# Kernel tuning notes

Hardware: AMD Instinct MI355X
Metric: run time of the kernel (lower is better)

Reference implementation:

```python
import jax, jax.numpy as jnp
import numpy as np

B, N, C, H = 2, 2048, 768, 12
D = C // H            # head_dim = 64
SCALE = D ** -0.5
QMAX_8 = 127.0        # int8 symmetric weights/activations (BIT_TYPE_W / BIT_TYPE_A)
LOG_QMAX = 15.0       # uint4 log-domain softmax (BIT_TYPE_S)


def setup_inputs() -> dict:
    key = jax.random.key(0)
    k0, k1, k2 = jax.random.split(key, 3)
    x = jax.random.normal(k0, (B, N, C), jnp.float32)
    w_qkv = jax.random.normal(k1, (3 * C, C), jnp.float32) * 0.02
    b_qkv = jnp.zeros((3 * C,), jnp.float32)
    w_out = jax.random.normal(k2, (C, C), jnp.float32) * 0.02
    b_out = jnp.zeros((C,), jnp.float32)
    return {"x": x, "w_qkv": w_qkv, "b_qkv": b_qkv, "w_out": w_out, "b_out": b_out}


def fake_quant_sym(t):
    """Symmetric per-tensor int8 fake-quantize (quantize->dequantize), STE for grads."""
    s = jnp.max(jnp.abs(t)) / QMAX_8 + 1e-8
    deq = jnp.clip(jnp.round(t / s), -QMAX_8, QMAX_8) * s
    return t + jax.lax.stop_gradient(deq - t)


def log_int_softmax(attn):
    """Log-int-softmax: softmax then 4-bit log2 quantization, attn_q = 2^{-round(-log2 p)}."""
    p = jax.nn.softmax(attn, axis=-1)
    lg = jnp.clip(jnp.round(-jnp.log2(jnp.maximum(p, 2.0 ** -24))), 0.0, LOG_QMAX)
    q = jnp.exp2(-lg)
    return p + jax.lax.stop_gradient(q - p)


def reference(x, w_qkv, b_qkv, w_out, b_out):
    # QLinear: fake-quantized weight GEMM
    qkv = x @ fake_quant_sym(w_qkv).T + b_qkv            # [B,N,3C]
    qkv = fake_quant_sym(qkv)                            # qact_qkv
    qkv = qkv.reshape(B, N, 3, H, D).transpose(2, 0, 3, 1, 4)  # [3,B,H,N,D]
    q, k, v = qkv[0], qkv[1], qkv[2]
    attn = jnp.einsum("bhnd,bhmd->bhnm", q, k) * SCALE   # [B,H,N,N]
    attn = fake_quant_sym(attn)                          # qact_attn
    p = log_int_softmax(attn)
    o = jnp.einsum("bhnm,bhmd->bhnd", p, v)              # [B,H,N,D]
    o = o.transpose(0, 2, 1, 3).reshape(B, N, C)
    out = o @ fake_quant_sym(w_out).T + b_out            # out_proj (QLinear)
    out = fake_quant_sym(out)                            # qact_out
    return out
```

## Files before the change

kernel.cpp:

```cpp
#include <hip/hip_runtime.h>

#define NB 2
#define NN 2048
#define NC 768
#define NH 12
#define ND 64
#define ROWS (NB * NN)
#define K3C (3 * NC)
#define NHEADS (NB * NH)
#define ATTN_SCALE 0.125f

typedef __attribute__((ext_vector_type(8))) short s16x8;
typedef __attribute__((ext_vector_type(4))) float f32x4;
typedef __attribute__((ext_vector_type(2))) unsigned int u32x2;

__device__ __forceinline__ float qsc(const unsigned* u) {
    return __uint_as_float(*u) / 127.0f + 1e-8f;
}
__device__ __forceinline__ float fq(float t, float s) {
    return fminf(fmaxf(rintf(t / s), -127.0f), 127.0f) * s;
}
__device__ __forceinline__ float qcode(float t, float s) {
    return fminf(fmaxf(rintf(t / s), -127.0f), 127.0f);
}
__device__ __forceinline__ short bfbits(float f) {
    return (short)(__float_as_uint(f) >> 16);
}
__device__ __forceinline__ ushort bf_rne(float x) {
    unsigned u = __float_as_uint(x);
    return (ushort)((u + 0x7fffu + ((u >> 16) & 1u)) >> 16);
}

__global__ __launch_bounds__(256) void maxabs_kernel(const float* __restrict__ x,
                                                     long long n, unsigned* out) {
    float m = 0.0f;
    long long stride4 = (long long)gridDim.x * blockDim.x * 4;
    for (long long j = ((long long)blockIdx.x * blockDim.x + threadIdx.x) * 4; j < n; j += stride4) {
        float4 v = *(const float4*)(x + j);
        m = fmaxf(m, fmaxf(fmaxf(fabsf(v.x), fabsf(v.y)), fmaxf(fabsf(v.z), fabsf(v.w))));
    }
    for (int off = 32; off > 0; off >>= 1) m = fmaxf(m, __shfl_down(m, off, 64));
    __shared__ float sm[4];
    int lane = threadIdx.x & 63, w = threadIdx.x >> 6;
    if (lane == 0) sm[w] = m;
    __syncthreads();
    if (threadIdx.x == 0) {
        float mm = fmaxf(fmaxf(sm[0], sm[1]), fmaxf(sm[2], sm[3]));
        atomicMax(out, __float_as_uint(mm));
    }
}

__global__ __launch_bounds__(256) void quant_kernel(const float* in, float* out,
                                                    long long n, const unsigned* umax) {
    float s = qsc(umax);
    long long stride4 = (long long)gridDim.x * blockDim.x * 4;
    for (long long j = ((long long)blockIdx.x * blockDim.x + threadIdx.x) * 4; j < n; j += stride4) {
        float4 v = *(const float4*)(in + j);
        v.x = fq(v.x, s); v.y = fq(v.y, s); v.z = fq(v.z, s); v.w = fq(v.w, s);
        *(float4*)(out + j) = v;
    }
}

__global__ __launch_bounds__(256) void quantcodes_kernel(const float* __restrict__ in,
                                                         ushort* __restrict__ codes,
                                                         long long n,
                                                         const unsigned* __restrict__ umax) {
    float s = qsc(umax);
    long long stride8 = (long long)gridDim.x * blockDim.x * 8;
    for (long long j = ((long long)blockIdx.x * blockDim.x + threadIdx.x) * 8; j < n; j += stride8) {
        float4 a = *(const float4*)(in + j);
        float4 b = *(const float4*)(in + j + 4);
        s16x8 o;
        o[0] = bfbits(qcode(a.x, s)); o[1] = bfbits(qcode(a.y, s));
        o[2] = bfbits(qcode(a.z, s)); o[3] = bfbits(qcode(a.w, s));
        o[4] = bfbits(qcode(b.x, s)); o[5] = bfbits(qcode(b.y, s));
        o[6] = bfbits(qcode(b.z, s)); o[7] = bfbits(qcode(b.w, s));
        *(s16x8*)(codes + j) = o;
    }
}

__global__ __launch_bounds__(256) void split3_kernel(const float* __restrict__ in,
                                                     ushort* __restrict__ xs,
                                                     long long n) {
    long long stride8 = (long long)gridDim.x * blockDim.x * 8;
    for (long long j = ((long long)blockIdx.x * blockDim.x + threadIdx.x) * 8; j < n; j += stride8) {
        long long row = j / NC, col = j % NC;
        s16x8 h, m, l;
#pragma unroll
        for (int i = 0; i < 8; i += 4) {
            float4 v = *(const float4*)(in + j + i);
            float vv[4] = {v.x, v.y, v.z, v.w};
#pragma unroll
            for (int t = 0; t < 4; ++t) {
                ushort hb = bf_rne(vv[t]);
                float hf = __uint_as_float(((unsigned)hb) << 16);
                float r1 = vv[t] - hf;
                ushort mb = bf_rne(r1);
                float mf = __uint_as_float(((unsigned)mb) << 16);
                h[i + t] = (short)hb;
                m[i + t] = (short)mb;
                l[i + t] = (short)bf_rne(r1 - mf);
            }
        }
        ushort* dst = xs + row * (3 * NC) + col;
        *(s16x8*)(dst) = h;
        *(s16x8*)(dst + NC) = m;
        *(s16x8*)(dst + 2 * NC) = l;
    }
}

__global__ __launch_bounds__(256) void gemm3_mfma_kernel(const ushort* __restrict__ As,
                                                         const ushort* __restrict__ Bc,
                                                         const float* __restrict__ bias,
                                                         float* __restrict__ Cm, int Nn,
                                                         const unsigned* __restrict__ uB,
                                                         unsigned* __restrict__ uC) {
    __shared__ ushort ah[128 * 64], am[128 * 64], al[128 * 64], bs[128 * 64];
    __shared__ float redmx[4];
    const float sB = qsc(uB);
    const int tid = threadIdx.x, l = tid & 63, w = tid >> 6;
    const int row0 = blockIdx.y * 128, col0 = blockIdx.x * 128;
    const int wr = w >> 1, wc = w & 1;
    f32x4 acc[4][4];
#pragma unroll
    for (int m = 0; m < 4; ++m)
#pragma unroll
        for (int n = 0; n < 4; ++n) acc[m][n] = (f32x4){0.f, 0.f, 0.f, 0.f};

    const int sr = tid >> 1, sh = (tid & 1) << 5;
    const int su = sh >> 3, s7 = sr & 7;

    for (int k0 = 0; k0 < NC; k0 += 64) {
        __syncthreads();
        {
            const ushort* ph = As + (size_t)(row0 + sr) * (3 * NC) + k0 + sh;
            ushort* dsts[3] = {ah + sr * 64, am + sr * 64, al + sr * 64};
#pragma unroll
            for (int pl = 0; pl < 3; ++pl) {
                const ushort* p = ph + pl * NC;
                s16x8 t0 = *(const s16x8*)(p),      t1 = *(const s16x8*)(p + 8);
                s16x8 t2 = *(const s16x8*)(p + 16), t3 = *(const s16x8*)(p + 24);
                ushort* d = dsts[pl];
                *(s16x8*)(d + (((su | 0) ^ s7) << 3)) = t0;
                *(s16x8*)(d + (((su | 1) ^ s7) << 3)) = t1;
                *(s16x8*)(d + (((su | 2) ^ s7) << 3)) = t2;
                *(s16x8*)(d + (((su | 3) ^ s7) << 3)) = t3;
            }
            const ushort* pb = Bc + (size_t)(col0 + sr) * NC + k0 + sh;
            s16x8 b0 = *(const s16x8*)(pb),      b1 = *(const s16x8*)(pb + 8);
            s16x8 b2 = *(const s16x8*)(pb + 16), b3 = *(const s16x8*)(pb + 24);
            ushort* brow = bs + sr * 64;
            *(s16x8*)(brow + (((su | 0) ^ s7) << 3)) = b0;
            *(s16x8*)(brow + (((su | 1) ^ s7) << 3)) = b1;
            *(s16x8*)(brow + (((su | 2) ^ s7) << 3)) = b2;
            *(s16x8*)(brow + (((su | 3) ^ s7) << 3)) = b3;
        }
        __syncthreads();
#pragma unroll
        for (int ks = 0; ks < 2; ++ks) {
            s16x8 bf[4];
#pragma unroll
            for (int n = 0; n < 4; ++n) {
                int br = wc * 64 + n * 16 + (l & 15);
                bf[n] = *(s16x8*)(bs + br * 64 + ((((ks << 2) + (l >> 4)) ^ (br & 7)) << 3));
            }
#pragma unroll
            for (int m = 0; m < 4; ++m) {
                int ar = wr * 64 + m * 16 + (l & 15);
                int ao = ar * 64 + ((((ks << 2) + (l >> 4)) ^ (ar & 7)) << 3);
                s16x8 af = *(s16x8*)(ah + ao);
                s16x8 mf_ = *(s16x8*)(am + ao);
                s16x8 ef = *(s16x8*)(al + ao);
#pragma unroll
                for (int n = 0; n < 4; ++n) {
                    acc[m][n] = __builtin_amdgcn_mfma_f32_16x16x32_bf16(af, bf[n], acc[m][n], 0, 0, 0);
                    acc[m][n] = __builtin_amdgcn_mfma_f32_16x16x32_bf16(mf_, bf[n], acc[m][n], 0, 0, 0);
                    acc[m][n] = __builtin_amdgcn_mfma_f32_16x16x32_bf16(ef, bf[n], acc[m][n], 0, 0, 0);
                }
            }
        }
    }
    float mx = 0.0f;
#pragma unroll
    for (int n = 0; n < 4; ++n) {
        int col = col0 + wc * 64 + n * 16 + (l & 15);
        float bv = bias[col];
#pragma unroll
        for (int m = 0; m < 4; ++m) {
            int grow = row0 + wr * 64 + m * 16 + ((l >> 4) << 2);
#pragma unroll
            for (int r = 0; r < 4; ++r) {
                float v = fmaf(sB, acc[m][n][r], bv);
                Cm[(size_t)(grow + r) * Nn + col] = v;
                mx = fmaxf(mx, fabsf(v));
            }
        }
    }
    for (int msk = 1; msk < 64; msk <<= 1) mx = fmaxf(mx, __shfl_xor(mx, msk, 64));
    if (l == 0) redmx[w] = mx;
    __syncthreads();
    if (tid == 0)
        atomicMax(uC, __float_as_uint(fmaxf(fmaxf(redmx[0], redmx[1]), fmaxf(redmx[2], redmx[3]))));
}

__device__ __forceinline__ void stage_k_tile(const ushort* __restrict__ src,
                                             ushort* lds, int tid) {
    int row = tid >> 2, u0 = (tid & 3) << 1, r7 = row & 7;
    const ushort* p = src + (size_t)row * K3C + (u0 << 3);
    s16x8 t0 = *(const s16x8*)(p);
    s16x8 t1 = *(const s16x8*)(p + 8);
    *(s16x8*)(lds + row * 64 + ((u0 ^ r7) << 3)) = t0;
    *(s16x8*)(lds + row * 64 + (((u0 | 1) ^ r7) << 3)) = t1;
}

__device__ __forceinline__ void stage_vT_tile(const ushort* __restrict__ src,
                                              ushort* lds, int tid) {
    int j = tid >> 2, d0 = (tid & 3) << 4;
    const ushort* p = src + (size_t)j * K3C + d0;
    s16x8 a = *(const s16x8*)(p);
    s16x8 b = *(const s16x8*)(p + 8);
    int jo = j >> 3, jl = j & 7;
#pragma unroll
    for (int t = 0; t < 8; ++t) {
        int d = d0 + t;
        lds[d * 64 + ((jo ^ (d & 7)) << 3) + jl] = (ushort)a[t];
    }
#pragma unroll
    for (int t = 0; t < 8; ++t) {
        int d = d0 + 8 + t;
        lds[d * 64 + ((jo ^ (d & 7)) << 3) + jl] = (ushort)b[t];
    }
}

__global__ __launch_bounds__(256) void attn_maxdot_kernel(const ushort* __restrict__ codes,
                                                          unsigned* __restrict__ umaxdot) {
    __shared__ ushort kt[64 * 64];
    __shared__ float red[4];
    int bh = blockIdx.y, b = bh / NH, h = bh % NH;
    int i0 = blockIdx.x * 64;
    int tid = threadIdx.x, l = tid & 63, w = tid >> 6;
    int qr = l & 15, g = l >> 4;

    const ushort* qp = codes + (size_t)(b * NN + i0 + w * 16 + qr) * K3C + h * ND + (g << 3);
    s16x8 qf0 = *(const s16x8*)(qp);
    s16x8 qf1 = *(const s16x8*)(qp + 32);

    const ushort* kbase = codes + (size_t)(b * NN) * K3C + NC + h * ND;
    float md = 0.0f;
    for (int st = 0; st < NN / 64; ++st) {
        __syncthreads();
        stage_k_tile(kbase + (size_t)st * 64 * K3C, kt, tid);
        __syncthreads();
#pragma unroll
        for (int jt = 0; jt < 4; ++jt) {
            int row = (jt << 4) + qr;
            f32x4 acc = {0.f, 0.f, 0.f, 0.f};
            s16x8 kf0 = *(s16x8*)(kt + row * 64 + (((g    ) ^ (row & 7)) << 3));
            s16x8 kf1 = *(s16x8*)(kt + row * 64 + (((g + 4) ^ (row & 7)) << 3));
            acc = __builtin_amdgcn_mfma_f32_16x16x32_bf16(kf0, qf0, acc, 0, 0, 0);
            acc = __builtin_amdgcn_mfma_f32_16x16x32_bf16(kf1, qf1, acc, 0, 0, 0);
#pragma unroll
            for (int r = 0; r < 4; ++r) md = fmaxf(md, fabsf(acc[r]));
        }
    }
    for (int m = 1; m < 64; m <<= 1) md = fmaxf(md, __shfl_xor(md, m, 64));
    if (l == 0) red[w] = md;
    __syncthreads();
    if (tid == 0)
        atomicMax(umaxdot, __float_as_uint(fmaxf(fmaxf(red[0], red[1]), fmaxf(red[2], red[3]))));
}

__global__ __launch_bounds__(256) void attn_fused_kernel(const ushort* __restrict__ codes,
                                                         const unsigned* __restrict__ uq,
                                                         const unsigned* __restrict__ umaxdot,
                                                         float* __restrict__ O) {
    __shared__ ushort kt[64 * 64];
    __shared__ ushort vt[64 * 64];
    __shared__ ushort ps[4][16 * 64];
    int bh = blockIdx.y, b = bh / NH, h = bh % NH;
    int i0 = blockIdx.x * 64;
    int tid = threadIdx.x, l = tid & 63, w = tid >> 6;
    int qr = l & 15, g = l >> 4;
    float s = qsc(uq);
    float cf = s * s * ATTN_SCALE;
    float sa = __uint_as_float(*umaxdot) * cf / 127.0f + 1e-8f;
    float rr = cf / sa;
    float kk = sa * 1.44269504088896340736f;

    const ushort* qp = codes + (size_t)(b * NN + i0 + w * 16 + qr) * K3C + h * ND + (g << 3);
    s16x8 qf0 = *(const s16x8*)(qp);
    s16x8 qf1 = *(const s16x8*)(qp + 32);

    const ushort* kbase = codes + (size_t)(b * NN) * K3C + NC + h * ND;
    const ushort* vbase = codes + (size_t)(b * NN) * K3C + 2 * NC + h * ND;

    float U = 0.0f;
    for (int st = 0; st < NN / 64; ++st) {
        __syncthreads();
        stage_k_tile(kbase + (size_t)st * 64 * K3C, kt, tid);
        __syncthreads();
#pragma unroll
        for (int jt = 0; jt < 4; ++jt) {
            int row = (jt << 4) + qr;
            f32x4 acc = {0.f, 0.f, 0.f, 0.f};
            s16x8 kf0 = *(s16x8*)(kt + row * 64 + (((g    ) ^ (row & 7)) << 3));
            s16x8 kf1 = *(s16x8*)(kt + row * 64 + (((g + 4) ^ (row & 7)) << 3));
            acc = __builtin_amdgcn_mfma_f32_16x16x32_bf16(kf0, qf0, acc, 0, 0, 0);
            acc = __builtin_amdgcn_mfma_f32_16x16x32_bf16(kf1, qf1, acc, 0, 0, 0);
#pragma unroll
            for (int r = 0; r < 4; ++r) {
                float m = rintf(acc[r] * rr);
                U += exp2f(kk * m);
            }
        }
    }
    U += __shfl_xor(U, 16, 64);
    U += __shfl_xor(U, 32, 64);
    float lu = log2f(U);

    f32x4 oacc[4];
#pragma unroll
    for (int dt = 0; dt < 4; ++dt) oacc[dt] = (f32x4){0.f, 0.f, 0.f, 0.f};
    ushort* myps = (ushort*)ps[w];
    for (int st = 0; st < NN / 64; ++st) {
        __syncthreads();
        stage_k_tile(kbase + (size_t)st * 64 * K3C, kt, tid);
        stage_vT_tile(vbase + (size_t)st * 64 * K3C, vt, tid);
        __syncthreads();
#pragma unroll
        for (int jt = 0; jt < 4; ++jt) {
            int row = (jt << 4) + qr;
            f32x4 acc = {0.f, 0.f, 0.f, 0.f};
            s16x8 kf0 = *(s16x8*)(kt + row * 64 + (((g    ) ^ (row & 7)) << 3));
            s16x8 kf1 = *(s16x8*)(kt + row * 64 + (((g + 4) ^ (row & 7)) << 3));
            acc = __builtin_amdgcn_mfma_f32_16x16x32_bf16(kf0, qf0, acc, 0, 0, 0);
            acc = __builtin_amdgcn_mfma_f32_16x16x32_bf16(kf1, qf1, acc, 0, 0, 0);
            int lg[4];
#pragma unroll
            for (int r = 0; r < 4; ++r) {
                float m = rintf(acc[r] * rr);
                float tt = lu - kk * m;
                lg[r] = (int)fminf(fmaxf(rintf(tt), 0.0f), 15.0f);
            }
            unsigned w0 = (unsigned)(((127 - lg[0]) << 7) | ((127 - lg[1]) << 23));
            unsigned w1 = (unsigned)(((127 - lg[2]) << 7) | ((127 - lg[3]) << 23));
            int off = qr * 64 + (((jt << 4) + ((g >> 1) << 3)) ^ ((qr & 7) << 3)) + ((g & 1) << 2);
            *(u32x2*)(myps + off) = (u32x2){w0, w1};
        }
#pragma unroll
        for (int kc = 0; kc < 2; ++kc) {
            int poff = qr * 64 + (((kc << 5) + (g << 3)) ^ ((qr & 7) << 3));
            s16x8 pf = *(s16x8*)(myps + poff);
#pragma unroll
            for (int dt = 0; dt < 4; ++dt) {
                int drow = (dt << 4) + qr;
                s16x8 vf = *(s16x8*)(vt + drow * 64 + ((((kc << 2) + g) ^ (drow & 7)) << 3));
                oacc[dt] = __builtin_amdgcn_mfma_f32_16x16x32_bf16(pf, vf, oacc[dt], 0, 0, 0);
            }
        }
    }
#pragma unroll
    for (int dt = 0; dt < 4; ++dt)
#pragma unroll
        for (int r = 0; r < 4; ++r) {
            int orow = i0 + w * 16 + (g << 2) + r;
            O[(size_t)(b * NN + orow) * NC + h * ND + (dt << 4) + qr] = s * oacc[dt][r];
        }
}

extern "C" void kernel_launch(void* const* d_in, const int* in_sizes, int n_in,
                              void* d_out, int out_size, void* d_ws, size_t ws_size,
                              hipStream_t stream) {
    const float* x      = (const float*)d_in[0];
    const float* w_qkv  = (const float*)d_in[1];
    const float* b_qkv  = (const float*)d_in[2];
    const float* w_out  = (const float*)d_in[3];
    const float* b_out  = (const float*)d_in[4];
    float* out = (float*)d_out;

    char* ws = (char*)d_ws;
    unsigned* u = (unsigned*)ws;
    const size_t qkvB = (size_t)ROWS * K3C * 4;
    float*  qkv     = (float*)(ws + 256);
    float*  out_tmp = (float*)(ws + 256);
    ushort* woc     = (ushort*)(ws + 256 + 16 * 1024 * 1024);
    char*   codesRg = ws + 256 + qkvB;
    ushort* codes   = (ushort*)codesRg;
    ushort* xsplit  = (ushort*)codesRg;
    ushort* wqc     = (ushort*)d_out;

    hipMemsetAsync(u, 0, 64, stream);

    maxabs_kernel<<<512, 256, 0, stream>>>(w_qkv, (long long)K3C * NC, u + 0);
    maxabs_kernel<<<512, 256, 0, stream>>>(w_out, (long long)NC * NC, u + 1);
    quantcodes_kernel<<<512, 256, 0, stream>>>(w_qkv, wqc, (long long)K3C * NC, u + 0);

    split3_kernel<<<1024, 256, 0, stream>>>(x, xsplit, (long long)ROWS * NC);
    gemm3_mfma_kernel<<<dim3(K3C / 128, ROWS / 128), 256, 0, stream>>>(xsplit, wqc, b_qkv,
                                                                       qkv, K3C, u + 0, u + 2);
    quantcodes_kernel<<<2048, 256, 0, stream>>>(qkv, codes, (long long)ROWS * K3C, u + 2);
    quantcodes_kernel<<<256, 256, 0, stream>>>(w_out, woc, (long long)NC * NC, u + 1);

    attn_maxdot_kernel<<<dim3(NN / 64, NHEADS), 256, 0, stream>>>(codes, u + 3);
    attn_fused_kernel<<<dim3(NN / 64, NHEADS), 256, 0, stream>>>(codes, u + 2, u + 3, out);

    split3_kernel<<<1024, 256, 0, stream>>>(out, xsplit, (long long)ROWS * NC);
    gemm3_mfma_kernel<<<dim3(NC / 128, ROWS / 128), 256, 0, stream>>>(xsplit, woc, b_out,
                                                                      out_tmp, NC, u + 1, u + 4);
    quant_kernel<<<1024, 256, 0, stream>>>(out_tmp, out, (long long)ROWS * NC, u + 4);
}
```

Measured before the change: 363.1 us.

## Pre-tile GEMM operands for direct global-to-LDS loads and drop K staging in attention

Split and quantize kernels now write their outputs in a pre-swizzled 64/128-row by 64-column tile layout. That lets a new GEMM kernel copy whole tiles into LDS with global_load_lds, using 64x128 tiles and a grouped block order. The attention kernels stop staging K in shared memory and read K fragments straight from global memory. The maxdot kernel shrinks to single-wave blocks with no barriers. These changes aim to cut register round-trips, barriers and LDS traffic. The cost is uncoalesced strided K reads, and the GEMM has no double buffering, so the DMA loads are not overlapped with compute.

```diff
diff --git a/kernel.cpp b/kernel.cpp
--- a/kernel.cpp
+++ b/kernel.cpp
@@ -8,6 +8,7 @@
 #define ROWS (NB * NN)
 #define K3C (3 * NC)
 #define NHEADS (NB * NH)
+#define NKB 12
 #define ATTN_SCALE 0.125f
 
 typedef __attribute__((ext_vector_type(8))) short s16x8;
@@ -29,6 +30,11 @@
 __device__ __forceinline__ ushort bf_rne(float x) {
     unsigned u = __float_as_uint(x);
     return (ushort)((u + 0x7fffu + ((u >> 16) & 1u)) >> 16);
+}
+__device__ __forceinline__ void glds16(const void* g, void* lds) {
+    __builtin_amdgcn_global_load_lds((const __attribute__((address_space(1))) unsigned int*)g,
+                                     (__attribute__((address_space(3))) unsigned int*)lds,
+                                     16, 0, 0);
 }
 
 __global__ __launch_bounds__(256) void maxabs_kernel(const float* __restrict__ x,
@@ -79,12 +85,36 @@
     }
 }
 
-__global__ __launch_bounds__(256) void split3_kernel(const float* __restrict__ in,
-                                                     ushort* __restrict__ xs,
-                                                     long long n) {
+__global__ __launch_bounds__(256) void quantcodes_tiled_kernel(const float* __restrict__ in,
+                                                               ushort* __restrict__ codes,
+                                                               long long n,
+                                                               const unsigned* __restrict__ umax) {
+    float s = qsc(umax);
     long long stride8 = (long long)gridDim.x * blockDim.x * 8;
     for (long long j = ((long long)blockIdx.x * blockDim.x + threadIdx.x) * 8; j < n; j += stride8) {
-        long long row = j / NC, col = j % NC;
+        long long r = j / NC;
+        int k = (int)(j % NC);
+        float4 a = *(const float4*)(in + j);
+        float4 b = *(const float4*)(in + j + 4);
+        s16x8 o;
+        o[0] = bfbits(qcode(a.x, s)); o[1] = bfbits(qcode(a.y, s));
+        o[2] = bfbits(qcode(a.z, s)); o[3] = bfbits(qcode(a.w, s));
+        o[4] = bfbits(qcode(b.x, s)); o[5] = bfbits(qcode(b.y, s));
+        o[6] = bfbits(qcode(b.z, s)); o[7] = bfbits(qcode(b.w, s));
+        int u = (k & 63) >> 3;
+        size_t dst = ((size_t)(r >> 7) * NKB + (k >> 6)) * 8192
+                   + (size_t)(r & 127) * 64 + (((u ^ (int)(r & 7))) << 3);
+        *(s16x8*)(codes + dst) = o;
+    }
+}
+
+__global__ __launch_bounds__(256) void split3_tiled_kernel(const float* __restrict__ in,
+                                                           ushort* __restrict__ xs,
+                                                           long long n) {
+    long long stride8 = (long long)gridDim.x * blockDim.x * 8;
+    for (long long j = ((long long)blockIdx.x * blockDim.x + threadIdx.x) * 8; j < n; j += stride8) {
+        long long r = j / NC;
+        int k = (int)(j % NC);
         s16x8 h, m, l;
 #pragma unroll
         for (int i = 0; i < 8; i += 4) {
@@ -102,95 +132,90 @@
                 l[i + t] = (short)bf_rne(r1 - mf);
             }
         }
-        ushort* dst = xs + row * (3 * NC) + col;
-        *(s16x8*)(dst) = h;
-        *(s16x8*)(dst + NC) = m;
-        *(s16x8*)(dst + 2 * NC) = l;
-    }
-}
-
-__global__ __launch_bounds__(256) void gemm3_mfma_kernel(const ushort* __restrict__ As,
-                                                         const ushort* __restrict__ Bc,
-                                                         const float* __restrict__ bias,
-                                                         float* __restrict__ Cm, int Nn,
-                                                         const unsigned* __restrict__ uB,
-                                                         unsigned* __restrict__ uC) {
-    __shared__ ushort ah[128 * 64], am[128 * 64], al[128 * 64], bs[128 * 64];
+        int u = (k & 63) >> 3;
+        size_t base = ((size_t)(r >> 6) * NKB + (k >> 6)) * 12288
+                    + (size_t)(r & 63) * 64 + (((u ^ (int)(r & 7))) << 3);
+        *(s16x8*)(xs + base) = h;
+        *(s16x8*)(xs + base + 4096) = m;
+        *(s16x8*)(xs + base + 8192) = l;
+    }
+}
+
+__global__ __launch_bounds__(256) void gemm_glds_kernel(const ushort* __restrict__ As,
+                                                        const ushort* __restrict__ Bc,
+                                                        const float* __restrict__ bias,
+                                                        float* __restrict__ Cm, int Nn,
+                                                        const unsigned* __restrict__ uB,
+                                                        unsigned* __restrict__ uC) {
+    __shared__ ushort aT[3 * 64 * 64];
+    __shared__ ushort bT[128 * 64];
     __shared__ float redmx[4];
     const float sB = qsc(uB);
     const int tid = threadIdx.x, l = tid & 63, w = tid >> 6;
-    const int row0 = blockIdx.y * 128, col0 = blockIdx.x * 128;
-    const int wr = w >> 1, wc = w & 1;
-    f32x4 acc[4][4];
+    const int nbx = Nn >> 7;
+    const int nwg = nbx * (ROWS / 64);
+    int bid = blockIdx.y * nbx + blockIdx.x;
+    int cpx = nwg >> 3;
+    int swz = (bid & 7) * cpx + (bid >> 3);
+    int bx = swz % nbx, by = swz / nbx;
+
+    f32x4 acc[4][2];
 #pragma unroll
     for (int m = 0; m < 4; ++m)
 #pragma unroll
-        for (int n = 0; n < 4; ++n) acc[m][n] = (f32x4){0.f, 0.f, 0.f, 0.f};
-
-    const int sr = tid >> 1, sh = (tid & 1) << 5;
-    const int su = sh >> 3, s7 = sr & 7;
-
-    for (int k0 = 0; k0 < NC; k0 += 64) {
+        for (int n = 0; n < 2; ++n) acc[m][n] = (f32x4){0.f, 0.f, 0.f, 0.f};
+
+    const char* tA = (const char*)As + (size_t)by * NKB * 24576;
+    const char* tB = (const char*)Bc + (size_t)bx * NKB * 16384;
+    const int lq = l & 15, lg = l >> 4;
+
+    for (int kb = 0; kb < NKB; ++kb) {
+#pragma unroll
+        for (int i = 0; i < 6; ++i)
+            glds16(tA + (size_t)i * 4096 + w * 1024 + l * 16,
+                   (char*)aT + i * 4096 + w * 1024);
+#pragma unroll
+        for (int i = 0; i < 4; ++i)
+            glds16(tB + (size_t)i * 4096 + w * 1024 + l * 16,
+                   (char*)bT + i * 4096 + w * 1024);
+        tA += 24576; tB += 16384;
         __syncthreads();
-        {
-            const ushort* ph = As + (size_t)(row0 + sr) * (3 * NC) + k0 + sh;
-            ushort* dsts[3] = {ah + sr * 64, am + sr * 64, al + sr * 64};
-#pragma unroll
-            for (int pl = 0; pl < 3; ++pl) {
-                const ushort* p = ph + pl * NC;
-                s16x8 t0 = *(const s16x8*)(p),      t1 = *(const s16x8*)(p + 8);
-                s16x8 t2 = *(const s16x8*)(p + 16), t3 = *(const s16x8*)(p + 24);
-                ushort* d = dsts[pl];
-                *(s16x8*)(d + (((su | 0) ^ s7) << 3)) = t0;
-                *(s16x8*)(d + (((su | 1) ^ s7) << 3)) = t1;
-                *(s16x8*)(d + (((su | 2) ^ s7) << 3)) = t2;
-                *(s16x8*)(d + (((su | 3) ^ s7) << 3)) = t3;
-            }
-            const ushort* pb = Bc + (size_t)(col0 + sr) * NC + k0 + sh;
-            s16x8 b0 = *(const s16x8*)(pb),      b1 = *(const s16x8*)(pb + 8);
-            s16x8 b2 = *(const s16x8*)(pb + 16), b3 = *(const s16x8*)(pb + 24);
-            ushort* brow = bs + sr * 64;
-            *(s16x8*)(brow + (((su | 0) ^ s7) << 3)) = b0;
-            *(s16x8*)(brow + (((su | 1) ^ s7) << 3)) = b1;
-            *(s16x8*)(brow + (((su | 2) ^ s7) << 3)) = b2;
-            *(s16x8*)(brow + (((su | 3) ^ s7) << 3)) = b3;
+#pragma unroll
+        for (int ks = 0; ks < 2; ++ks) {
+            s16x8 bf[2];
+#pragma unroll
+            for (int nf = 0; nf < 2; ++nf) {
+                int br = w * 32 + nf * 16 + lq;
+                bf[nf] = *(s16x8*)(bT + br * 64 + ((((ks << 2) + lg) ^ (br & 7)) << 3));
+            }
+#pragma unroll
+            for (int m = 0; m < 4; ++m) {
+                int ar = m * 16 + lq;
+                int ao = ar * 64 + ((((ks << 2) + lg) ^ (ar & 7)) << 3);
+                s16x8 af = *(s16x8*)(aT + ao);
+                s16x8 mf_ = *(s16x8*)(aT + 4096 + ao);
+                s16x8 ef = *(s16x8*)(aT + 8192 + ao);
+#pragma unroll
+                for (int nf = 0; nf < 2; ++nf) {
+                    acc[m][nf] = __builtin_amdgcn_mfma_f32_16x16x32_bf16(af, bf[nf], acc[m][nf], 0, 0, 0);
+                    acc[m][nf] = __builtin_amdgcn_mfma_f32_16x16x32_bf16(mf_, bf[nf], acc[m][nf], 0, 0, 0);
+                    acc[m][nf] = __builtin_amdgcn_mfma_f32_16x16x32_bf16(ef, bf[nf], acc[m][nf], 0, 0, 0);
+                }
+            }
         }
         __syncthreads();
-#pragma unroll
-        for (int ks = 0; ks < 2; ++ks) {
-            s16x8 bf[4];
-#pragma unroll
-            for (int n = 0; n < 4; ++n) {
-                int br = wc * 64 + n * 16 + (l & 15);
-                bf[n] = *(s16x8*)(bs + br * 64 + ((((ks << 2) + (l >> 4)) ^ (br & 7)) << 3));
-            }
-#pragma unroll
-            for (int m = 0; m < 4; ++m) {
-                int ar = wr * 64 + m * 16 + (l & 15);
-                int ao = ar * 64 + ((((ks << 2) + (l >> 4)) ^ (ar & 7)) << 3);
-                s16x8 af = *(s16x8*)(ah + ao);
-                s16x8 mf_ = *(s16x8*)(am + ao);
-                s16x8 ef = *(s16x8*)(al + ao);
-#pragma unroll
-                for (int n = 0; n < 4; ++n) {
-                    acc[m][n] = __builtin_amdgcn_mfma_f32_16x16x32_bf16(af, bf[n], acc[m][n], 0, 0, 0);
-                    acc[m][n] = __builtin_amdgcn_mfma_f32_16x16x32_bf16(mf_, bf[n], acc[m][n], 0, 0, 0);
-                    acc[m][n] = __builtin_amdgcn_mfma_f32_16x16x32_bf16(ef, bf[n], acc[m][n], 0, 0, 0);
-                }
-            }
-        }
     }
     float mx = 0.0f;
 #pragma unroll
-    for (int n = 0; n < 4; ++n) {
-        int col = col0 + wc * 64 + n * 16 + (l & 15);
+    for (int nf = 0; nf < 2; ++nf) {
+        int col = bx * 128 + w * 32 + nf * 16 + lq;
         float bv = bias[col];
 #pragma unroll
         for (int m = 0; m < 4; ++m) {
-            int grow = row0 + wr * 64 + m * 16 + ((l >> 4) << 2);
+            int grow = by * 64 + m * 16 + (lg << 2);
 #pragma unroll
             for (int r = 0; r < 4; ++r) {
-                float v = fmaf(sB, acc[m][n][r], bv);
+                float v = fmaf(sB, acc[m][nf][r], bv);
                 Cm[(size_t)(grow + r) * Nn + col] = v;
                 mx = fmaxf(mx, fabsf(v));
             }
@@ -201,16 +226,6 @@
     __syncthreads();
     if (tid == 0)
         atomicMax(uC, __float_as_uint(fmaxf(fmaxf(redmx[0], redmx[1]), fmaxf(redmx[2], redmx[3]))));
-}
-
-__device__ __forceinline__ void stage_k_tile(const ushort* __restrict__ src,
-                                             ushort* lds, int tid) {
-    int row = tid >> 2, u0 = (tid & 3) << 1, r7 = row & 7;
-    const ushort* p = src + (size_t)row * K3C + (u0 << 3);
-    s16x8 t0 = *(const s16x8*)(p);
-    s16x8 t1 = *(const s16x8*)(p + 8);
-    *(s16x8*)(lds + row * 64 + ((u0 ^ r7) << 3)) = t0;
-    *(s16x8*)(lds + row * 64 + (((u0 | 1) ^ r7) << 3)) = t1;
 }
 
 __device__ __forceinline__ void stage_vT_tile(const ushort* __restrict__ src,
@@ -232,31 +247,25 @@
     }
 }
 
-__global__ __launch_bounds__(256) void attn_maxdot_kernel(const ushort* __restrict__ codes,
-                                                          unsigned* __restrict__ umaxdot) {
-    __shared__ ushort kt[64 * 64];
-    __shared__ float red[4];
+__global__ __launch_bounds__(64) void attn_maxdot_kernel(const ushort* __restrict__ codes,
+                                                         unsigned* __restrict__ umaxdot) {
     int bh = blockIdx.y, b = bh / NH, h = bh % NH;
-    int i0 = blockIdx.x * 64;
-    int tid = threadIdx.x, l = tid & 63, w = tid >> 6;
-    int qr = l & 15, g = l >> 4;
-
-    const ushort* qp = codes + (size_t)(b * NN + i0 + w * 16 + qr) * K3C + h * ND + (g << 3);
+    int i0 = blockIdx.x << 4;
+    int l = threadIdx.x, qr = l & 15, g = l >> 4;
+
+    const ushort* qp = codes + (size_t)(b * NN + i0 + qr) * K3C + h * ND + (g << 3);
     s16x8 qf0 = *(const s16x8*)(qp);
     s16x8 qf1 = *(const s16x8*)(qp + 32);
 
-    const ushort* kbase = codes + (size_t)(b * NN) * K3C + NC + h * ND;
+    const ushort* kl = codes + ((size_t)b * NN + qr) * K3C + NC + h * ND + (g << 3);
     float md = 0.0f;
     for (int st = 0; st < NN / 64; ++st) {
-        __syncthreads();
-        stage_k_tile(kbase + (size_t)st * 64 * K3C, kt, tid);
-        __syncthreads();
+        const ushort* kt0 = kl + (size_t)st * 64 * K3C;
 #pragma unroll
         for (int jt = 0; jt < 4; ++jt) {
-            int row = (jt << 4) + qr;
+            s16x8 kf0 = *(const s16x8*)(kt0 + (size_t)jt * 16 * K3C);
+            s16x8 kf1 = *(const s16x8*)(kt0 + (size_t)jt * 16 * K3C + 32);
             f32x4 acc = {0.f, 0.f, 0.f, 0.f};
-            s16x8 kf0 = *(s16x8*)(kt + row * 64 + (((g    ) ^ (row & 7)) << 3));
-            s16x8 kf1 = *(s16x8*)(kt + row * 64 + (((g + 4) ^ (row & 7)) << 3));
             acc = __builtin_amdgcn_mfma_f32_16x16x32_bf16(kf0, qf0, acc, 0, 0, 0);
             acc = __builtin_amdgcn_mfma_f32_16x16x32_bf16(kf1, qf1, acc, 0, 0, 0);
 #pragma unroll
@@ -264,17 +273,13 @@
         }
     }
     for (int m = 1; m < 64; m <<= 1) md = fmaxf(md, __shfl_xor(md, m, 64));
-    if (l == 0) red[w] = md;
-    __syncthreads();
-    if (tid == 0)
-        atomicMax(umaxdot, __float_as_uint(fmaxf(fmaxf(red[0], red[1]), fmaxf(red[2], red[3]))));
+    if (l == 0) atomicMax(umaxdot, __float_as_uint(md));
 }
 
 __global__ __launch_bounds__(256) void attn_fused_kernel(const ushort* __restrict__ codes,
                                                          const unsigned* __restrict__ uq,
                                                          const unsigned* __restrict__ umaxdot,
                                                          float* __restrict__ O) {
-    __shared__ ushort kt[64 * 64];
     __shared__ ushort vt[64 * 64];
     __shared__ ushort ps[4][16 * 64];
     int bh = blockIdx.y, b = bh / NH, h = bh % NH;
@@ -291,20 +296,17 @@
     s16x8 qf0 = *(const s16x8*)(qp);
     s16x8 qf1 = *(const s16x8*)(qp + 32);
 
-    const ushort* kbase = codes + (size_t)(b * NN) * K3C + NC + h * ND;
+    const ushort* kl = codes + ((size_t)b * NN + qr) * K3C + NC + h * ND + (g << 3);
     const ushort* vbase = codes + (size_t)(b * NN) * K3C + 2 * NC + h * ND;
 
     float U = 0.0f;
     for (int st = 0; st < NN / 64; ++st) {
-        __syncthreads();
-        stage_k_tile(kbase + (size_t)st * 64 * K3C, kt, tid);
-        __syncthreads();
+        const ushort* kt0 = kl + (size_t)st * 64 * K3C;
 #pragma unroll
         for (int jt = 0; jt < 4; ++jt) {
-            int row = (jt << 4) + qr;
+            s16x8 kf0 = *(const s16x8*)(kt0 + (size_t)jt * 16 * K3C);
+            s16x8 kf1 = *(const s16x8*)(kt0 + (size_t)jt * 16 * K3C + 32);
             f32x4 acc = {0.f, 0.f, 0.f, 0.f};
-            s16x8 kf0 = *(s16x8*)(kt + row * 64 + (((g    ) ^ (row & 7)) << 3));
-            s16x8 kf1 = *(s16x8*)(kt + row * 64 + (((g + 4) ^ (row & 7)) << 3));
             acc = __builtin_amdgcn_mfma_f32_16x16x32_bf16(kf0, qf0, acc, 0, 0, 0);
             acc = __builtin_amdgcn_mfma_f32_16x16x32_bf16(kf1, qf1, acc, 0, 0, 0);
 #pragma unroll
@@ -324,15 +326,14 @@
     ushort* myps = (ushort*)ps[w];
     for (int st = 0; st < NN / 64; ++st) {
         __syncthreads();
-        stage_k_tile(kbase + (size_t)st * 64 * K3C, kt, tid);
         stage_vT_tile(vbase + (size_t)st * 64 * K3C, vt, tid);
         __syncthreads();
+        const ushort* kt0 = kl + (size_t)st * 64 * K3C;
 #pragma unroll
         for (int jt = 0; jt < 4; ++jt) {
-            int row = (jt << 4) + qr;
+            s16x8 kf0 = *(const s16x8*)(kt0 + (size_t)jt * 16 * K3C);
+            s16x8 kf1 = *(const s16x8*)(kt0 + (size_t)jt * 16 * K3C + 32);
             f32x4 acc = {0.f, 0.f, 0.f, 0.f};
-            s16x8 kf0 = *(s16x8*)(kt + row * 64 + (((g    ) ^ (row & 7)) << 3));
-            s16x8 kf1 = *(s16x8*)(kt + row * 64 + (((g + 4) ^ (row & 7)) << 3));
             acc = __builtin_amdgcn_mfma_f32_16x16x32_bf16(kf0, qf0, acc, 0, 0, 0);
             acc = __builtin_amdgcn_mfma_f32_16x16x32_bf16(kf1, qf1, acc, 0, 0, 0);
             int lg[4];
@@ -393,19 +394,19 @@
 
     maxabs_kernel<<<512, 256, 0, stream>>>(w_qkv, (long long)K3C * NC, u + 0);
     maxabs_kernel<<<512, 256, 0, stream>>>(w_out, (long long)NC * NC, u + 1);
-    quantcodes_kernel<<<512, 256, 0, stream>>>(w_qkv, wqc, (long long)K3C * NC, u + 0);
-
-    split3_kernel<<<1024, 256, 0, stream>>>(x, xsplit, (long long)ROWS * NC);
-    gemm3_mfma_kernel<<<dim3(K3C / 128, ROWS / 128), 256, 0, stream>>>(xsplit, wqc, b_qkv,
-                                                                       qkv, K3C, u + 0, u + 2);
+    quantcodes_tiled_kernel<<<512, 256, 0, stream>>>(w_qkv, wqc, (long long)K3C * NC, u + 0);
+
+    split3_tiled_kernel<<<1024, 256, 0, stream>>>(x, xsplit, (long long)ROWS * NC);
+    gemm_glds_kernel<<<dim3(K3C / 128, ROWS / 64), 256, 0, stream>>>(xsplit, wqc, b_qkv,
+                                                                     qkv, K3C, u + 0, u + 2);
     quantcodes_kernel<<<2048, 256, 0, stream>>>(qkv, codes, (long long)ROWS * K3C, u + 2);
-    quantcodes_kernel<<<256, 256, 0, stream>>>(w_out, woc, (long long)NC * NC, u + 1);
-
-    attn_maxdot_kernel<<<dim3(NN / 64, NHEADS), 256, 0, stream>>>(codes, u + 3);
+    quantcodes_tiled_kernel<<<256, 256, 0, stream>>>(w_out, woc, (long long)NC * NC, u + 1);
+
+    attn_maxdot_kernel<<<dim3(NN / 16, NHEADS), 64, 0, stream>>>(codes, u + 3);
     attn_fused_kernel<<<dim3(NN / 64, NHEADS), 256, 0, stream>>>(codes, u + 2, u + 3, out);
 
-    split3_kernel<<<1024, 256, 0, stream>>>(out, xsplit, (long long)ROWS * NC);
-    gemm3_mfma_kernel<<<dim3(NC / 128, ROWS / 128), 256, 0, stream>>>(xsplit, woc, b_out,
-                                                                      out_tmp, NC, u + 1, u + 4);
+    split3_tiled_kernel<<<1024, 256, 0, stream>>>(out, xsplit, (long long)ROWS * NC);
+    gemm_glds_kernel<<<dim3(NC / 128, ROWS / 64), 256, 0, stream>>>(xsplit, woc, b_out,
+                                                                    out_tmp, NC, u + 1, u + 4);
     quant_kernel<<<1024, 256, 0, stream>>>(out_tmp, out, (long long)ROWS * NC, u + 4);
 }
```

Result: slower. 491.1 us (+35.2%).
